# Optimization experiments

Measured on AMD Instinct MI355X. Metric: run time of the kernel, lower is better.

Reference implementation:

```python
import jax, jax.numpy as jnp
import numpy as np
import math

B, T, D, H, L = 64, 255, 512, 8, 8
CODEBOOK = 512
V = CODEBOOK + 3  # bos/eos/pad
COND_DIM = 512
MAX_LEN = 256
HD = D // H


def _layernorm(x, g, b, eps=1e-5):
    mu = jnp.mean(x, axis=-1, keepdims=True)
    var = jnp.mean(jnp.square(x - mu), axis=-1, keepdims=True)
    return (x - mu) * jax.lax.rsqrt(var + eps) * g + b


def setup_inputs() -> dict:
    key = jax.random.key(0)
    ks = jax.random.split(key, 24)
    s = 0.02
    d = {
        'tokens': jax.random.randint(ks[0], (B, T), 0, V),
        'cond': jax.random.normal(ks[1], (B, COND_DIM), jnp.float32),
        'emb': jax.random.normal(ks[2], (V, D), jnp.float32) * s,  # tied token_emb / head weight
        'pos_emb': jax.random.normal(ks[3], (1, MAX_LEN, D), jnp.float32) * s,
        'cond_w1': jax.random.normal(ks[4], (COND_DIM, D), jnp.float32) * s,
        'cond_b1': jnp.zeros((D,), jnp.float32),
        'cond_w2': jax.random.normal(ks[5], (D, D), jnp.float32) * s,
        'cond_b2': jnp.zeros((D,), jnp.float32),
        'ln1_g': jnp.ones((L, D), jnp.float32),
        'ln1_b': jnp.zeros((L, D), jnp.float32),
        'qkv_w': jax.random.normal(ks[6], (L, D, 3 * D), jnp.float32) * s,
        'qkv_b': jnp.zeros((L, 3 * D), jnp.float32),
        'proj_w': jax.random.normal(ks[7], (L, D, D), jnp.float32) * s,
        'proj_b': jnp.zeros((L, D), jnp.float32),
        'ln2_g': jnp.ones((L, D), jnp.float32),
        'ln2_b': jnp.zeros((L, D), jnp.float32),
        'mlp_w1': jax.random.normal(ks[8], (L, D, 4 * D), jnp.float32) * s,
        'mlp_b1': jnp.zeros((L, 4 * D), jnp.float32),
        'mlp_w2': jax.random.normal(ks[9], (L, 4 * D, D), jnp.float32) * s,
        'mlp_b2': jnp.zeros((L, D), jnp.float32),
        'lnf_g': jnp.ones((D,), jnp.float32),
        'lnf_b': jnp.zeros((D,), jnp.float32),
    }
    return d


def reference(tokens, cond, emb, pos_emb, cond_w1, cond_b1, cond_w2, cond_b2,
              ln1_g, ln1_b, qkv_w, qkv_b, proj_w, proj_b,
              ln2_g, ln2_b, mlp_w1, mlp_b1, mlp_w2, mlp_b2, lnf_g, lnf_b):
    b, t = tokens.shape
    h = emb[tokens] + pos_emb[:, :t, :]                              # [B,T,D]
    c = jax.nn.silu(cond @ cond_w1 + cond_b1) @ cond_w2 + cond_b2    # [B,D]
    h = jnp.concatenate([c[:, None, :], h], axis=1)                  # [B,S,D]
    S = t + 1
    causal = jnp.tril(jnp.ones((S, S), bool))
    scale = 1.0 / math.sqrt(HD)
    for i in range(L):
        x = _layernorm(h, ln1_g[i], ln1_b[i])
        qkv = (x @ qkv_w[i] + qkv_b[i]).reshape(b, S, 3, H, HD).transpose(2, 0, 3, 1, 4)
        q, k, v = qkv[0], qkv[1], qkv[2]                             # [B,H,S,hd]
        a = jnp.einsum('bhsd,bhtd->bhst', q, k) * scale
        a = jnp.where(causal, a, -jnp.inf)
        a = jax.nn.softmax(a, axis=-1)
        o = jnp.einsum('bhst,bhtd->bhsd', a, v).transpose(0, 2, 1, 3).reshape(b, S, D)
        h = h + o @ proj_w[i] + proj_b[i]
        x = _layernorm(h, ln2_g[i], ln2_b[i])
        h = h + jax.nn.gelu(x @ mlp_w1[i] + mlp_b1[i], approximate=False) @ mlp_w2[i] + mlp_b2[i]
    h = _layernorm(h, lnf_g, lnf_b)
    return (h @ emb.T)[:, 1:, :]                                     # [B,T,V]
```

## Files before the change

### kernel.cpp

```cpp
#include <hip/hip_runtime.h>
#include <hip/hip_bf16.h>

typedef __attribute__((ext_vector_type(8))) short bf16x8;
typedef __attribute__((ext_vector_type(4))) float f32x4;
typedef __attribute__((ext_vector_type(4))) unsigned short u16x4;
typedef __attribute__((ext_vector_type(8))) unsigned short u16x8;
typedef unsigned short u16;

#define DEV static __device__ __forceinline__

DEV float bf2f(u16 u) {
  union { unsigned int i; float f; } c; c.i = ((unsigned int)u) << 16; return c.f;
}
DEV u16 f2bf(float f) {
  union { float f; unsigned int i; } c; c.f = f;
  unsigned int i = c.i;
  i += 0x7FFFu + ((i >> 16) & 1u);
  return (u16)(i >> 16);
}

DEV void gload_lds16(const void* g, void* l) {
  __builtin_amdgcn_global_load_lds((const __attribute__((address_space(1))) void*)g,
                                   (__attribute__((address_space(3))) void*)l, 16, 0, 0);
}

DEV f32x4 mfma16(bf16x8 a, bf16x8 b, f32x4 c) {
  return __builtin_amdgcn_mfma_f32_16x16x32_bf16(a, b, c, 0, 0, 0);
}

DEV float fasterf(float x) {
  float ax = fabsf(x);
  float t = 1.0f / (1.0f + 0.3275911f * ax);
  float y = t * (0.254829592f + t * (-0.284496736f + t * (1.421413741f +
            t * (-1.453152027f + t * 1.061405429f))));
  float r = 1.0f - y * __expf(-ax * ax);
  return copysignf(r, x);
}
DEV float gelu(float v) { return 0.5f * v * (1.0f + fasterf(v * 0.70710678118f)); }

__global__ __launch_bounds__(256) void ktranspose(const float* __restrict__ in, u16* __restrict__ out,
                                                  int K, int N) {
  __shared__ u16 tile[32][33];
  const float* src = in + (size_t)blockIdx.z * K * N;
  u16* dst = out + (size_t)blockIdx.z * K * N;
  const int n0 = blockIdx.x * 32, k0 = blockIdx.y * 32;
  const int tx = threadIdx.x, ty = threadIdx.y;
#pragma unroll
  for (int i = ty; i < 32; i += 8) tile[i][tx] = f2bf(src[(size_t)(k0 + i) * N + n0 + tx]);
  __syncthreads();
#pragma unroll
  for (int i = ty; i < 32; i += 8) dst[(size_t)(n0 + i) * K + k0 + tx] = tile[tx][i];
}

__global__ __launch_bounds__(256) void kcvt(const float* __restrict__ in, u16* __restrict__ out, int n) {
  int i = blockIdx.x * 256 + threadIdx.x;
  if (i < n) out[i] = f2bf(in[i]);
}

__global__ __launch_bounds__(256) void kcond(const float* __restrict__ cond, const float* __restrict__ w1,
                                             const float* __restrict__ b1, const float* __restrict__ w2,
                                             const float* __restrict__ b2, float* __restrict__ h) {
  __shared__ float xr[512];
  __shared__ float t1[512];
  const int b = blockIdx.x, tid = threadIdx.x;
  for (int i = tid; i < 512; i += 256) xr[i] = cond[b * 512 + i];
  __syncthreads();
  for (int j = tid; j < 512; j += 256) {
    float acc = b1[j];
    for (int k = 0; k < 512; ++k) acc += xr[k] * w1[k * 512 + j];
    t1[j] = acc / (1.f + __expf(-acc));
  }
  __syncthreads();
  for (int j = tid; j < 512; j += 256) {
    float acc = b2[j];
    for (int k = 0; k < 512; ++k) acc += t1[k] * w2[k * 512 + j];
    h[(size_t)b * 256 * 512 + j] = acc;
  }
}

__global__ __launch_bounds__(256) void kembed(const int* __restrict__ tok, const float* __restrict__ emb,
                                              const float* __restrict__ pos, float* __restrict__ h) {
  const int idx = blockIdx.x;
  const int b = idx / 255, t = idx % 255;
  const int c = threadIdx.x * 2;
  const int tk = tok[idx];
  float2 ev = *(const float2*)(emb + (size_t)tk * 512 + c);
  float2 pv = *(const float2*)(pos + (size_t)t * 512 + c);
  float2 r;
  r.x = ev.x + pv.x;
  r.y = ev.y + pv.y;
  *(float2*)(h + ((size_t)b * 256 + 1 + t) * 512 + c) = r;
}

__global__ __launch_bounds__(256) void kln(const float* __restrict__ hin, const float* __restrict__ g,
                                           const float* __restrict__ bt, u16* __restrict__ out) {
  const int row = blockIdx.x * 4 + (threadIdx.x >> 6), lane = threadIdx.x & 63;
  const float4* x = (const float4*)(hin + (size_t)row * 512);
  float4 v0 = x[lane], v1 = x[lane + 64];
  float s1 = v0.x + v0.y + v0.z + v0.w + v1.x + v1.y + v1.z + v1.w;
  float s2 = v0.x * v0.x + v0.y * v0.y + v0.z * v0.z + v0.w * v0.w +
             v1.x * v1.x + v1.y * v1.y + v1.z * v1.z + v1.w * v1.w;
#pragma unroll
  for (int off = 1; off < 64; off <<= 1) { s1 += __shfl_xor(s1, off); s2 += __shfl_xor(s2, off); }
  float mu = s1 * (1.f / 512.f);
  float var = s2 * (1.f / 512.f) - mu * mu;
  float rs = rsqrtf(var + 1e-5f);
  const int c0 = lane * 4;
  float4 g0 = *(const float4*)(g + c0), g1 = *(const float4*)(g + 256 + c0);
  float4 b0 = *(const float4*)(bt + c0), b1 = *(const float4*)(bt + 256 + c0);
  u16x4 o0, o1;
  o0[0] = f2bf((v0.x - mu) * rs * g0.x + b0.x);
  o0[1] = f2bf((v0.y - mu) * rs * g0.y + b0.y);
  o0[2] = f2bf((v0.z - mu) * rs * g0.z + b0.z);
  o0[3] = f2bf((v0.w - mu) * rs * g0.w + b0.w);
  o1[0] = f2bf((v1.x - mu) * rs * g1.x + b1.x);
  o1[1] = f2bf((v1.y - mu) * rs * g1.y + b1.y);
  o1[2] = f2bf((v1.z - mu) * rs * g1.z + b1.z);
  o1[3] = f2bf((v1.w - mu) * rs * g1.w + b1.w);
  *(u16x4*)(out + (size_t)row * 512 + c0) = o0;
  *(u16x4*)(out + (size_t)row * 512 + 256 + c0) = o1;
}

template<int MODE>
__global__ __launch_bounds__(256, 2) void kgemm3(const u16* __restrict__ A, const u16* __restrict__ Bt,
                                                 const float* __restrict__ bias, void* __restrict__ Cout,
                                                 int M, int N, int K) {
  __shared__ __align__(16) u16 As[3][4096];
  __shared__ __align__(16) u16 Bs[3][4096];
  const int tid = threadIdx.x;
  const int lane = tid & 63;
  const int wr = tid >> 7, wc = (tid >> 6) & 1;
  const int m0 = blockIdx.x * 128, n0 = blockIdx.y * 128;
  const int nkt = K >> 5;
  const size_t Kb = (size_t)K * 2;

  const int srow = tid >> 2;
  const int schunk = tid & 3;
  const int sc = schunk ^ ((srow >> 1) & 3);
  const int d1 = tid * 16, d2 = tid * 16 + 4096;
  int brA = n0 + srow, brB = n0 + srow + 64;
  if (MODE == 3) { brA = min(brA, N - 1); brB = min(brB, N - 1); }
  const char* Ab = (const char*)A;
  const char* Bb = (const char*)Bt;
  const size_t a0 = (size_t)(m0 + srow) * Kb + sc * 16;
  const size_t a1 = (size_t)(m0 + srow + 64) * Kb + sc * 16;
  const size_t b0 = (size_t)brA * Kb + sc * 16;
  const size_t b1 = (size_t)brB * Kb + sc * 16;

  f32x4 acc[4][4];
#pragma unroll
  for (int i = 0; i < 4; ++i)
#pragma unroll
    for (int j = 0; j < 4; ++j) acc[i][j] = f32x4{0.f, 0.f, 0.f, 0.f};

#pragma unroll
  for (int t = 0; t < 2; ++t) {
    const size_t ko = (size_t)t * 64;
    gload_lds16(Ab + a0 + ko, (char*)As[t] + d1);
    gload_lds16(Ab + a1 + ko, (char*)As[t] + d2);
    gload_lds16(Bb + b0 + ko, (char*)Bs[t] + d1);
    gload_lds16(Bb + b1 + ko, (char*)Bs[t] + d2);
  }
  asm volatile("s_waitcnt vmcnt(4)" ::: "memory");
  __builtin_amdgcn_s_barrier();
  __builtin_amdgcn_sched_barrier(0);

  const int kchunk = (((lane >> 4) ^ ((lane >> 1) & 3)) << 4);
  const int arow = wr * 64 + (lane & 15);
  const int brow = wc * 64 + (lane & 15);

  for (int kt = 0; kt < nkt; ++kt) {
    const int bufc = kt % 3;
    const bool deep = (kt + 2 < nkt);
    if (deep) {
      const int bufn = (kt + 2) % 3;
      const size_t ko = (size_t)(kt + 2) * 64;
      gload_lds16(Ab + a0 + ko, (char*)As[bufn] + d1);
      gload_lds16(Ab + a1 + ko, (char*)As[bufn] + d2);
      gload_lds16(Bb + b0 + ko, (char*)Bs[bufn] + d1);
      gload_lds16(Bb + b1 + ko, (char*)Bs[bufn] + d2);
    }
    const char* Ap = (const char*)As[bufc];
    const char* Bp = (const char*)Bs[bufc];
    bf16x8 aF[4], bF[4];
#pragma unroll
    for (int mt = 0; mt < 4; ++mt) aF[mt] = *(const bf16x8*)(Ap + (arow + mt * 16) * 64 + kchunk);
#pragma unroll
    for (int nt = 0; nt < 4; ++nt) bF[nt] = *(const bf16x8*)(Bp + (brow + nt * 16) * 64 + kchunk);
#pragma unroll
    for (int mt = 0; mt < 4; ++mt)
#pragma unroll
      for (int nt = 0; nt < 4; ++nt)
        acc[mt][nt] = mfma16(aF[mt], bF[nt], acc[mt][nt]);
    if (deep) {
      asm volatile("s_waitcnt vmcnt(4)" ::: "memory");
    } else {
      asm volatile("s_waitcnt vmcnt(0)" ::: "memory");
    }
    __builtin_amdgcn_s_barrier();
    __builtin_amdgcn_sched_barrier(0);
  }

  float bv[4];
#pragma unroll
  for (int nt = 0; nt < 4; ++nt) {
    int col = n0 + wc * 64 + nt * 16 + (lane & 15);
    bv[nt] = (MODE == 3) ? 0.f : bias[col];
  }

  if (MODE == 0 || MODE == 1) {
    u16* C = (u16*)Cout;
#pragma unroll
    for (int mt = 0; mt < 4; ++mt)
#pragma unroll
      for (int r = 0; r < 4; ++r) {
        int row = m0 + wr * 64 + mt * 16 + (lane >> 4) * 4 + r;
        u16* cp = C + (size_t)row * N + n0 + wc * 64 + (lane & 15);
#pragma unroll
        for (int nt = 0; nt < 4; ++nt) {
          float v = acc[mt][nt][r] + bv[nt];
          if (MODE == 1) v = gelu(v);
          cp[nt * 16] = f2bf(v);
        }
      }
  } else if (MODE == 2) {
    float* hC = (float*)Cout;
#pragma unroll
    for (int mt = 0; mt < 4; ++mt)
#pragma unroll
      for (int r = 0; r < 4; ++r) {
        int row = m0 + wr * 64 + mt * 16 + (lane >> 4) * 4 + r;
        float* hp = hC + (size_t)row * N + n0 + wc * 64 + (lane & 15);
#pragma unroll
        for (int nt = 0; nt < 4; ++nt) hp[nt * 16] += acc[mt][nt][r] + bv[nt];
      }
  } else {
    float* C = (float*)Cout;
#pragma unroll
    for (int mt = 0; mt < 4; ++mt)
#pragma unroll
      for (int r = 0; r < 4; ++r) {
        int row = m0 + wr * 64 + mt * 16 + (lane >> 4) * 4 + r;
        int s = row & 255;
        if (s == 0) continue;
        int bb = row >> 8;
        float* cp = C + ((size_t)bb * 255 + (s - 1)) * 515 + n0 + wc * 64 + (lane & 15);
#pragma unroll
        for (int nt = 0; nt < 4; ++nt) {
          int col = n0 + wc * 64 + nt * 16 + (lane & 15);
          if (col < 515) cp[nt * 16] = acc[mt][nt][r];
        }
      }
  }
}

__global__ __launch_bounds__(256, 1) void kattn(const u16* __restrict__ qkv, u16* __restrict__ o) {
  __shared__ __align__(16) u16 Ks[256][72];
  __shared__ __align__(16) u16 Vt[64][264];
  __shared__ __align__(16) u16 Ps[4][64][72];
  const int tid = threadIdx.x, wv = tid >> 6, lane = tid & 63;
  const int bh = blockIdx.x, bb = bh >> 3, hh = bh & 7;
  const size_t base = (size_t)bb * 256 * 1536 + hh * 64;

  for (int c = tid; c < 2048; c += 256) {
    int s = c >> 3, pp = c & 7;
    u16x8 kv = *(const u16x8*)(qkv + base + (size_t)s * 1536 + 512 + pp * 8);
    *(u16x8*)&Ks[s][pp * 8] = kv;
    u16x8 vv = *(const u16x8*)(qkv + base + (size_t)s * 1536 + 1024 + pp * 8);
#pragma unroll
    for (int j = 0; j < 8; ++j) Vt[pp * 8 + j][s] = vv[j];
  }
  __syncthreads();

  bf16x8 qf[4][2];
#pragma unroll
  for (int mt = 0; mt < 4; ++mt)
#pragma unroll
    for (int ks = 0; ks < 2; ++ks)
      qf[mt][ks] = *(const bf16x8*)(qkv + base +
                   (size_t)(wv * 64 + mt * 16 + (lane & 15)) * 1536 + ks * 32 + (lane >> 4) * 8);

  const float scale = 0.125f;
  float mrow[4][4], lsum[4][4];
#pragma unroll
  for (int mt = 0; mt < 4; ++mt)
#pragma unroll
    for (int r = 0; r < 4; ++r) { mrow[mt][r] = -1e30f; lsum[mt][r] = 0.f; }

  for (int ct = 0; ct <= wv; ++ct) {
    f32x4 sacc[4][4];
#pragma unroll
    for (int i = 0; i < 4; ++i)
#pragma unroll
      for (int j = 0; j < 4; ++j) sacc[i][j] = f32x4{0.f, 0.f, 0.f, 0.f};
#pragma unroll
    for (int ks = 0; ks < 2; ++ks) {
      bf16x8 kf[4];
#pragma unroll
      for (int nt = 0; nt < 4; ++nt)
        kf[nt] = *(const bf16x8*)&Ks[ct * 64 + nt * 16 + (lane & 15)][ks * 32 + (lane >> 4) * 8];
#pragma unroll
      for (int mt = 0; mt < 4; ++mt)
#pragma unroll
        for (int nt = 0; nt < 4; ++nt)
          sacc[mt][nt] = mfma16(qf[mt][ks], kf[nt], sacc[mt][nt]);
    }
#pragma unroll
    for (int mt = 0; mt < 4; ++mt)
#pragma unroll
      for (int r = 0; r < 4; ++r) {
        int srow = wv * 64 + mt * 16 + (lane >> 4) * 4 + r;
        float mx = -1e30f;
#pragma unroll
        for (int nt = 0; nt < 4; ++nt) {
          int tcol = ct * 64 + nt * 16 + (lane & 15);
          float v = sacc[mt][nt][r] * scale;
          if (tcol > srow) v = -1e30f;
          mx = fmaxf(mx, v);
        }
#pragma unroll
        for (int off = 1; off < 16; off <<= 1) mx = fmaxf(mx, __shfl_xor(mx, off));
        mrow[mt][r] = fmaxf(mrow[mt][r], mx);
      }
  }

  f32x4 oacc[4][4];
#pragma unroll
  for (int i = 0; i < 4; ++i)
#pragma unroll
    for (int j = 0; j < 4; ++j) oacc[i][j] = f32x4{0.f, 0.f, 0.f, 0.f};

  for (int ct = 0; ct <= wv; ++ct) {
    f32x4 sacc[4][4];
#pragma unroll
    for (int i = 0; i < 4; ++i)
#pragma unroll
      for (int j = 0; j < 4; ++j) sacc[i][j] = f32x4{0.f, 0.f, 0.f, 0.f};
#pragma unroll
    for (int ks = 0; ks < 2; ++ks) {
      bf16x8 kf[4];
#pragma unroll
      for (int nt = 0; nt < 4; ++nt)
        kf[nt] = *(const bf16x8*)&Ks[ct * 64 + nt * 16 + (lane & 15)][ks * 32 + (lane >> 4) * 8];
#pragma unroll
      for (int mt = 0; mt < 4; ++mt)
#pragma unroll
        for (int nt = 0; nt < 4; ++nt)
          sacc[mt][nt] = mfma16(qf[mt][ks], kf[nt], sacc[mt][nt]);
    }
#pragma unroll
    for (int mt = 0; mt < 4; ++mt)
#pragma unroll
      for (int r = 0; r < 4; ++r) {
        int srow = wv * 64 + mt * 16 + (lane >> 4) * 4 + r;
        float ps = 0.f;
#pragma unroll
        for (int nt = 0; nt < 4; ++nt) {
          int tcol = ct * 64 + nt * 16 + (lane & 15);
          float v = sacc[mt][nt][r] * scale;
          float pe = (tcol > srow) ? 0.f : __expf(v - mrow[mt][r]);
          ps += pe;
          Ps[wv][mt * 16 + (lane >> 4) * 4 + r][nt * 16 + (lane & 15)] = f2bf(pe);
        }
#pragma unroll
        for (int off = 1; off < 16; off <<= 1) ps += __shfl_xor(ps, off);
        lsum[mt][r] += ps;
      }
#pragma unroll
    for (int ks = 0; ks < 2; ++ks) {
      bf16x8 pf[4], vf[4];
#pragma unroll
      for (int mt = 0; mt < 4; ++mt)
        pf[mt] = *(const bf16x8*)&Ps[wv][mt * 16 + (lane & 15)][ks * 32 + (lane >> 4) * 8];
#pragma unroll
      for (int nt = 0; nt < 4; ++nt)
        vf[nt] = *(const bf16x8*)&Vt[nt * 16 + (lane & 15)][ct * 64 + ks * 32 + (lane >> 4) * 8];
#pragma unroll
      for (int mt = 0; mt < 4; ++mt)
#pragma unroll
        for (int nt = 0; nt < 4; ++nt)
          oacc[mt][nt] = mfma16(pf[mt], vf[nt], oacc[mt][nt]);
    }
  }

#pragma unroll
  for (int mt = 0; mt < 4; ++mt)
#pragma unroll
    for (int r = 0; r < 4; ++r) {
      int s = wv * 64 + mt * 16 + (lane >> 4) * 4 + r;
      float inv = 1.f / lsum[mt][r];
      u16* op = o + ((size_t)bb * 256 + s) * 512 + hh * 64 + (lane & 15);
#pragma unroll
      for (int nt = 0; nt < 4; ++nt) op[nt * 16] = f2bf(oacc[mt][nt][r] * inv);
    }
}

extern "C" void kernel_launch(void* const* d_in, const int* in_sizes, int n_in,
                              void* d_out, int out_size, void* d_ws, size_t ws_size,
                              hipStream_t stream) {
  const int* tokens = (const int*)d_in[0];
  const float* cond = (const float*)d_in[1];
  const float* emb = (const float*)d_in[2];
  const float* pos = (const float*)d_in[3];
  const float* cw1 = (const float*)d_in[4];
  const float* cb1 = (const float*)d_in[5];
  const float* cw2 = (const float*)d_in[6];
  const float* cb2 = (const float*)d_in[7];
  const float* ln1g = (const float*)d_in[8];
  const float* ln1b = (const float*)d_in[9];
  const float* qkvw = (const float*)d_in[10];
  const float* qkvb = (const float*)d_in[11];
  const float* projw = (const float*)d_in[12];
  const float* projb = (const float*)d_in[13];
  const float* ln2g = (const float*)d_in[14];
  const float* ln2b = (const float*)d_in[15];
  const float* w1 = (const float*)d_in[16];
  const float* b1 = (const float*)d_in[17];
  const float* w2 = (const float*)d_in[18];
  const float* b2 = (const float*)d_in[19];
  const float* lnfg = (const float*)d_in[20];
  const float* lnfb = (const float*)d_in[21];

  const size_t NEEDED = (size_t)16384 * 512 * 4
                      + (size_t)16384 * 512 * 2
                      + (size_t)16384 * 2048 * 2
                      + (size_t)8 * 1536 * 512 * 2
                      + (size_t)8 * 512 * 512 * 2
                      + (size_t)8 * 2048 * 512 * 2
                      + (size_t)8 * 512 * 2048 * 2;
  if (ws_size < NEEDED) return;

  char* p = (char*)d_ws;
  float* h = (float*)p;        p += (size_t)16384 * 512 * 4;
  u16* xln = (u16*)p;          p += (size_t)16384 * 512 * 2;
  u16* big = (u16*)p;          p += (size_t)16384 * 2048 * 2;
  u16* attn_o = big + (size_t)16384 * 1536;
  u16* embB = big;
  u16* qkvT = (u16*)p;         p += (size_t)8 * 1536 * 512 * 2;
  u16* projT = (u16*)p;        p += (size_t)8 * 512 * 512 * 2;
  u16* w1T = (u16*)p;          p += (size_t)8 * 2048 * 512 * 2;
  u16* w2T = (u16*)p;          p += (size_t)8 * 512 * 2048 * 2;

  ktranspose<<<dim3(48, 16, 8), dim3(32, 8), 0, stream>>>(qkvw, qkvT, 512, 1536);
  ktranspose<<<dim3(16, 16, 8), dim3(32, 8), 0, stream>>>(projw, projT, 512, 512);
  ktranspose<<<dim3(64, 16, 8), dim3(32, 8), 0, stream>>>(w1, w1T, 512, 2048);
  ktranspose<<<dim3(16, 64, 8), dim3(32, 8), 0, stream>>>(w2, w2T, 2048, 512);

  kembed<<<16320, 256, 0, stream>>>(tokens, emb, pos, h);
  kcond<<<64, 256, 0, stream>>>(cond, cw1, cb1, cw2, cb2, h);

  for (int l = 0; l < 8; ++l) {
    kln<<<4096, 256, 0, stream>>>(h, ln1g + l * 512, ln1b + l * 512, xln);
    kgemm3<0><<<dim3(128, 12), 256, 0, stream>>>(xln, qkvT + (size_t)l * 1536 * 512,
                                                 qkvb + l * 1536, big, 16384, 1536, 512);
    kattn<<<512, 256, 0, stream>>>(big, attn_o);
    kgemm3<2><<<dim3(128, 4), 256, 0, stream>>>(attn_o, projT + (size_t)l * 512 * 512,
                                                projb + l * 512, h, 16384, 512, 512);
    kln<<<4096, 256, 0, stream>>>(h, ln2g + l * 512, ln2b + l * 512, xln);
    kgemm3<1><<<dim3(128, 16), 256, 0, stream>>>(xln, w1T + (size_t)l * 2048 * 512,
                                                 b1 + l * 2048, big, 16384, 2048, 512);
    kgemm3<2><<<dim3(128, 4), 256, 0, stream>>>(big, w2T + (size_t)l * 512 * 2048,
                                                b2 + l * 512, h, 16384, 512, 2048);
  }
  kln<<<4096, 256, 0, stream>>>(h, lnfg, lnfb, xln);
  kcvt<<<1030, 256, 0, stream>>>(emb, embB, 515 * 512);
  kgemm3<3><<<dim3(128, 5), 256, 0, stream>>>(xln, embB, nullptr, d_out, 16384, 515, 512);
}
```

Measured before the change: 2.104 ms.

## Fuse residual GEMMs with LayerNorm, single-pass attention, tanh GELU

Adds a kgemmln kernel where each block owns 64 full rows of the 512-wide output. It adds bias and residual, writes h, and computes the next LayerNorm in place, so the separate kln launches and their reread of h go away. Attention moves from a two-pass max-then-exp scheme to an online softmax that rescales running sums and accumulators, so QK^T is computed once instead of twice. The erf-based GELU becomes the tanh approximation, which is cheaper but differs numerically from the exact GELU the reference uses. The fused GEMM has only 256 blocks with wide N tiles, which may lower occupancy or parallelism.

```diff
diff --git a/kernel.cpp b/kernel.cpp
--- a/kernel.cpp
+++ b/kernel.cpp
@@ -28,15 +28,14 @@
   return __builtin_amdgcn_mfma_f32_16x16x32_bf16(a, b, c, 0, 0, 0);
 }
 
-DEV float fasterf(float x) {
-  float ax = fabsf(x);
-  float t = 1.0f / (1.0f + 0.3275911f * ax);
-  float y = t * (0.254829592f + t * (-0.284496736f + t * (1.421413741f +
-            t * (-1.453152027f + t * 1.061405429f))));
-  float r = 1.0f - y * __expf(-ax * ax);
-  return copysignf(r, x);
-}
-DEV float gelu(float v) { return 0.5f * v * (1.0f + fasterf(v * 0.70710678118f)); }
+template<int N> DEV void vwait() { asm volatile("s_waitcnt vmcnt(%0)" :: "n"(N) : "memory"); }
+
+DEV float gelu(float x) {
+  float t2 = __builtin_fmaf(0.044715f * x * x, x, x);
+  float e = __expf(1.5957691216f * t2);
+  float th = 1.f - 2.f / (e + 1.f);
+  return 0.5f * x * (1.f + th);
+}
 
 __global__ __launch_bounds__(256) void ktranspose(const float* __restrict__ in, u16* __restrict__ out,
                                                   int K, int N) {
@@ -223,17 +222,6 @@
           cp[nt * 16] = f2bf(v);
         }
       }
-  } else if (MODE == 2) {
-    float* hC = (float*)Cout;
-#pragma unroll
-    for (int mt = 0; mt < 4; ++mt)
-#pragma unroll
-      for (int r = 0; r < 4; ++r) {
-        int row = m0 + wr * 64 + mt * 16 + (lane >> 4) * 4 + r;
-        float* hp = hC + (size_t)row * N + n0 + wc * 64 + (lane & 15);
-#pragma unroll
-        for (int nt = 0; nt < 4; ++nt) hp[nt * 16] += acc[mt][nt][r] + bv[nt];
-      }
   } else {
     float* C = (float*)Cout;
 #pragma unroll
@@ -252,6 +240,129 @@
         }
       }
   }
+}
+
+__global__ __launch_bounds__(256, 2) void kgemmln(const u16* __restrict__ A, const u16* __restrict__ Bt,
+                                                  const float* __restrict__ bias, float* __restrict__ h,
+                                                  const float* __restrict__ g, const float* __restrict__ be,
+                                                  u16* __restrict__ xln, int K) {
+  __shared__ __align__(16) u16 As[2][2048];
+  __shared__ __align__(16) u16 Bs[2][16384];
+  __shared__ float redS[64][4];
+  __shared__ float redQ[64][4];
+  const int tid = threadIdx.x, lane = tid & 63, w = tid >> 6;
+  const int fr = lane & 15, fq = lane >> 4;
+  const int m0 = blockIdx.x * 64;
+  const int nkt = K >> 5;
+  const size_t Kb = (size_t)K * 2;
+  const char* Ab = (const char*)A;
+  const char* Bb = (const char*)Bt;
+
+  const int sarow = tid >> 2;
+  const size_t aSrc = (size_t)(m0 + sarow) * Kb + (((tid & 3) ^ ((sarow >> 1) & 3)) << 4);
+  const int aDst = tid * 16;
+  size_t bSrc[8];
+  int bDst[8];
+#pragma unroll
+  for (int j = 0; j < 8; ++j) {
+    int d = tid * 16 + j * 4096;
+    int row = d >> 6, chk = (d >> 4) & 3;
+    bSrc[j] = (size_t)row * Kb + ((chk ^ ((row >> 1) & 3)) << 4);
+    bDst[j] = d;
+  }
+
+  f32x4 acc[4][8];
+#pragma unroll
+  for (int i = 0; i < 4; ++i)
+#pragma unroll
+    for (int j = 0; j < 8; ++j) acc[i][j] = f32x4{0.f, 0.f, 0.f, 0.f};
+
+  gload_lds16(Ab + aSrc, (char*)As[0] + aDst);
+#pragma unroll
+  for (int j = 0; j < 8; ++j) gload_lds16(Bb + bSrc[j], (char*)Bs[0] + bDst[j]);
+  asm volatile("s_waitcnt vmcnt(0)" ::: "memory");
+  __builtin_amdgcn_s_barrier();
+  __builtin_amdgcn_sched_barrier(0);
+
+  const int kchunk = (((lane >> 4) ^ ((lane >> 1) & 3)) << 4);
+
+  for (int kt = 0; kt < nkt; ++kt) {
+    const int buf = kt & 1;
+    const bool more = (kt + 1 < nkt);
+    if (more) {
+      const size_t ko = (size_t)(kt + 1) * 64;
+      gload_lds16(Ab + aSrc + ko, (char*)As[buf ^ 1] + aDst);
+#pragma unroll
+      for (int j = 0; j < 8; ++j) gload_lds16(Bb + bSrc[j] + ko, (char*)Bs[buf ^ 1] + bDst[j]);
+    }
+    const char* Ap = (const char*)As[buf];
+    const char* Bp = (const char*)Bs[buf];
+    bf16x8 aF[4], bF[8];
+#pragma unroll
+    for (int m = 0; m < 4; ++m) aF[m] = *(const bf16x8*)(Ap + (m * 16 + fr) * 64 + kchunk);
+#pragma unroll
+    for (int n = 0; n < 8; ++n) bF[n] = *(const bf16x8*)(Bp + (w * 128 + n * 16 + fr) * 64 + kchunk);
+#pragma unroll
+    for (int m = 0; m < 4; ++m)
+#pragma unroll
+      for (int n = 0; n < 8; ++n)
+        acc[m][n] = mfma16(aF[m], bF[n], acc[m][n]);
+    if (more) {
+      asm volatile("s_waitcnt vmcnt(0)" ::: "memory");
+      __builtin_amdgcn_s_barrier();
+      __builtin_amdgcn_sched_barrier(0);
+    }
+  }
+
+  float bv[8], gv[8], bev[8];
+#pragma unroll
+  for (int n = 0; n < 8; ++n) {
+    int col = w * 128 + n * 16 + fr;
+    bv[n] = bias[col];
+    gv[n] = g[col];
+    bev[n] = be[col];
+  }
+#pragma unroll
+  for (int m = 0; m < 4; ++m)
+#pragma unroll
+    for (int r = 0; r < 4; ++r) {
+      int lrow = m * 16 + fq * 4 + r;
+      size_t rowb = (size_t)(m0 + lrow) * 512;
+      float s = 0.f, q = 0.f;
+#pragma unroll
+      for (int n = 0; n < 8; ++n) {
+        float hv = h[rowb + w * 128 + n * 16 + fr];
+        float val = acc[m][n][r] + bv[n] + hv;
+        acc[m][n][r] = val;
+        s += val;
+        q += val * val;
+      }
+#pragma unroll
+      for (int off = 1; off < 16; off <<= 1) { s += __shfl_xor(s, off); q += __shfl_xor(q, off); }
+      if (fr == 0) { redS[lrow][w] = s; redQ[lrow][w] = q; }
+    }
+  __syncthreads();
+#pragma unroll
+  for (int m = 0; m < 4; ++m)
+#pragma unroll
+    for (int r = 0; r < 4; ++r) {
+      int lrow = m * 16 + fq * 4 + r;
+      float4 s4 = *(const float4*)redS[lrow];
+      float4 q4 = *(const float4*)redQ[lrow];
+      float sum = s4.x + s4.y + s4.z + s4.w;
+      float qq = q4.x + q4.y + q4.z + q4.w;
+      float mu = sum * (1.f / 512.f);
+      float var = qq * (1.f / 512.f) - mu * mu;
+      float rs = rsqrtf(var + 1e-5f);
+      size_t rowb = (size_t)(m0 + lrow) * 512;
+#pragma unroll
+      for (int n = 0; n < 8; ++n) {
+        int col = w * 128 + n * 16 + fr;
+        float val = acc[m][n][r];
+        h[rowb + col] = val;
+        xln[rowb + col] = f2bf((val - mu) * rs * gv[n] + bev[n]);
+      }
+    }
 }
 
 __global__ __launch_bounds__(256, 1) void kattn(const u16* __restrict__ qkv, u16* __restrict__ o) {
@@ -287,6 +398,12 @@
 #pragma unroll
     for (int r = 0; r < 4; ++r) { mrow[mt][r] = -1e30f; lsum[mt][r] = 0.f; }
 
+  f32x4 oacc[4][4];
+#pragma unroll
+  for (int i = 0; i < 4; ++i)
+#pragma unroll
+    for (int j = 0; j < 4; ++j) oacc[i][j] = f32x4{0.f, 0.f, 0.f, 0.f};
+
   for (int ct = 0; ct <= wv; ++ct) {
     f32x4 sacc[4][4];
 #pragma unroll
@@ -310,61 +427,32 @@
 #pragma unroll
       for (int r = 0; r < 4; ++r) {
         int srow = wv * 64 + mt * 16 + (lane >> 4) * 4 + r;
+        float v[4];
         float mx = -1e30f;
 #pragma unroll
         for (int nt = 0; nt < 4; ++nt) {
           int tcol = ct * 64 + nt * 16 + (lane & 15);
-          float v = sacc[mt][nt][r] * scale;
-          if (tcol > srow) v = -1e30f;
-          mx = fmaxf(mx, v);
+          float vv = sacc[mt][nt][r] * scale;
+          v[nt] = (tcol > srow) ? -1e30f : vv;
+          mx = fmaxf(mx, v[nt]);
         }
 #pragma unroll
         for (int off = 1; off < 16; off <<= 1) mx = fmaxf(mx, __shfl_xor(mx, off));
-        mrow[mt][r] = fmaxf(mrow[mt][r], mx);
-      }
-  }
-
-  f32x4 oacc[4][4];
-#pragma unroll
-  for (int i = 0; i < 4; ++i)
-#pragma unroll
-    for (int j = 0; j < 4; ++j) oacc[i][j] = f32x4{0.f, 0.f, 0.f, 0.f};
-
-  for (int ct = 0; ct <= wv; ++ct) {
-    f32x4 sacc[4][4];
-#pragma unroll
-    for (int i = 0; i < 4; ++i)
-#pragma unroll
-      for (int j = 0; j < 4; ++j) sacc[i][j] = f32x4{0.f, 0.f, 0.f, 0.f};
-#pragma unroll
-    for (int ks = 0; ks < 2; ++ks) {
-      bf16x8 kf[4];
-#pragma unroll
-      for (int nt = 0; nt < 4; ++nt)
-        kf[nt] = *(const bf16x8*)&Ks[ct * 64 + nt * 16 + (lane & 15)][ks * 32 + (lane >> 4) * 8];
-#pragma unroll
-      for (int mt = 0; mt < 4; ++mt)
-#pragma unroll
-        for (int nt = 0; nt < 4; ++nt)
-          sacc[mt][nt] = mfma16(qf[mt][ks], kf[nt], sacc[mt][nt]);
-    }
-#pragma unroll
-    for (int mt = 0; mt < 4; ++mt)
-#pragma unroll
-      for (int r = 0; r < 4; ++r) {
-        int srow = wv * 64 + mt * 16 + (lane >> 4) * 4 + r;
+        float mnew = fmaxf(mrow[mt][r], mx);
+        float sf = __expf(mrow[mt][r] - mnew);
+        mrow[mt][r] = mnew;
         float ps = 0.f;
 #pragma unroll
         for (int nt = 0; nt < 4; ++nt) {
-          int tcol = ct * 64 + nt * 16 + (lane & 15);
-          float v = sacc[mt][nt][r] * scale;
-          float pe = (tcol > srow) ? 0.f : __expf(v - mrow[mt][r]);
+          float pe = (v[nt] <= -1e29f) ? 0.f : __expf(v[nt] - mnew);
           ps += pe;
           Ps[wv][mt * 16 + (lane >> 4) * 4 + r][nt * 16 + (lane & 15)] = f2bf(pe);
         }
 #pragma unroll
         for (int off = 1; off < 16; off <<= 1) ps += __shfl_xor(ps, off);
-        lsum[mt][r] += ps;
+        lsum[mt][r] = lsum[mt][r] * sf + ps;
+#pragma unroll
+        for (int nt = 0; nt < 4; ++nt) oacc[mt][nt][r] *= sf;
       }
 #pragma unroll
     for (int ks = 0; ks < 2; ++ks) {
@@ -448,21 +536,21 @@
 
   kembed<<<16320, 256, 0, stream>>>(tokens, emb, pos, h);
   kcond<<<64, 256, 0, stream>>>(cond, cw1, cb1, cw2, cb2, h);
+  kln<<<4096, 256, 0, stream>>>(h, ln1g, ln1b, xln);
 
   for (int l = 0; l < 8; ++l) {
-    kln<<<4096, 256, 0, stream>>>(h, ln1g + l * 512, ln1b + l * 512, xln);
     kgemm3<0><<<dim3(128, 12), 256, 0, stream>>>(xln, qkvT + (size_t)l * 1536 * 512,
                                                  qkvb + l * 1536, big, 16384, 1536, 512);
     kattn<<<512, 256, 0, stream>>>(big, attn_o);
-    kgemm3<2><<<dim3(128, 4), 256, 0, stream>>>(attn_o, projT + (size_t)l * 512 * 512,
-                                                projb + l * 512, h, 16384, 512, 512);
-    kln<<<4096, 256, 0, stream>>>(h, ln2g + l * 512, ln2b + l * 512, xln);
+    kgemmln<<<256, 256, 0, stream>>>(attn_o, projT + (size_t)l * 512 * 512, projb + l * 512,
+                                     h, ln2g + l * 512, ln2b + l * 512, xln, 512);
     kgemm3<1><<<dim3(128, 16), 256, 0, stream>>>(xln, w1T + (size_t)l * 2048 * 512,
                                                  b1 + l * 2048, big, 16384, 2048, 512);
-    kgemm3<2><<<dim3(128, 4), 256, 0, stream>>>(big, w2T + (size_t)l * 512 * 2048,
-                                                b2 + l * 512, h, 16384, 512, 2048);
-  }
-  kln<<<4096, 256, 0, stream>>>(h, lnfg, lnfb, xln);
+    const float* ng = (l < 7) ? (ln1g + (l + 1) * 512) : lnfg;
+    const float* nb = (l < 7) ? (ln1b + (l + 1) * 512) : lnfb;
+    kgemmln<<<256, 256, 0, stream>>>(big, w2T + (size_t)l * 512 * 2048, b2 + l * 512,
+                                     h, ng, nb, xln, 2048);
+  }
   kcvt<<<1030, 256, 0, stream>>>(emb, embB, 515 * 512);
   kgemm3<3><<<dim3(128, 5), 256, 0, stream>>>(xln, embB, nullptr, d_out, 16384, 515, 512);
 }
```

Result: slower. 2.360 ms (+12.2%).
